# Kernel tuning notes

Measured on AMD Instinct MI355X. Metric: run time of the kernel, lower is better.

The kernel has to match this reference:

```python
import jax, jax.numpy as jnp
import numpy as np

H, W = 192, 640  # image feature-map size (x_rgb[0].shape[2:])


def _pts2img(coor, feat):
    """coor: [N,2] normalized (u,v) in [0,1]; feat: [N,C] -> [C,H,W].
    Mirrors pts2img: swap to (v,u), scale by (H,W), truncate to int,
    last-write-wins scatter into (H+1,W+1,C), crop the overflow row/col."""
    coor = jnp.clip(coor, 0.0, 1.0)
    rc = (coor[:, ::-1] * jnp.array([H, W], coor.dtype)).astype(jnp.int32)  # [N,2] (row,col)
    grid = jnp.zeros((H + 1, W + 1, feat.shape[1]), feat.dtype)
    grid = grid.at[rc[:, 0], rc[:, 1]].set(feat)
    return grid[:H, :W].transpose(2, 0, 1)  # [C,H,W]


def _conv1x1(x, Wm, b):
    # x: [B,C,H,W], Wm: [O,C]
    return jnp.einsum('bchw,oc->bohw', x, Wm) + b[None, :, None, None]


def _conv3x3(x, Wk, b):
    y = jax.lax.conv_general_dilated(x, Wk, window_strides=(1, 1),
                                     padding=((1, 1), (1, 1)),
                                     dimension_numbers=('NCHW', 'OIHW', 'NCHW'))
    return y + b[None, :, None, None]


def setup_inputs() -> dict:
    key = jax.random.key(0)
    ks = jax.random.split(key, 16)
    B, C_IMG = 2, 64
    N0, C0 = 40000, 32
    N1, C1 = 20000, 64
    CL = C1 + 3  # 67
    s = 0.05
    return {
        'x_rgb0': jax.random.normal(ks[0], (B, C_IMG, H, W), jnp.float32),
        'feat0': jax.random.normal(ks[1], (B, N0, C0), jnp.float32),
        'coor0': jax.random.uniform(ks[2], (B, N0, 2), jnp.float32),
        'vox0': jax.random.normal(ks[3], (B, N0, 3), jnp.float32),
        'feat1': jax.random.normal(ks[4], (B, N1, C1), jnp.float32),
        'coor1': jax.random.uniform(ks[5], (B, N1, 2), jnp.float32),
        'vox1': jax.random.normal(ks[6], (B, N1, 3), jnp.float32),
        'W_red0': s * jax.random.normal(ks[7], (CL, C0 + 3), jnp.float32),
        'b_red0': s * jax.random.normal(ks[8], (CL,), jnp.float32),
        'W_red2': s * jax.random.normal(ks[9], (CL, CL), jnp.float32),
        'b_red2': s * jax.random.normal(ks[10], (CL,), jnp.float32),
        'W_red3': s * jax.random.normal(ks[11], (1, C_IMG), jnp.float32),
        'b_red3': s * jax.random.normal(ks[12], (1,), jnp.float32),
        'W_sp': s * jax.random.normal(ks[13], (1, CL, 3, 3), jnp.float32),
        'b_sp': s * jax.random.normal(ks[14], (1,), jnp.float32),
    }


def reference(x_rgb0, feat0, coor0, vox0, feat1, coor1, vox1,
              W_red0, b_red0, W_red2, b_red2, W_red3, b_red3, W_sp, b_sp):
    scatter = jax.vmap(_pts2img)  # over batch
    # level features = cat(sparse features, 3D voxel coords)
    pts_img0 = scatter(coor0, jnp.concatenate([feat0, vox0], axis=-1))  # [B,35,H,W]
    pts_img1 = scatter(coor1, jnp.concatenate([feat1, vox1], axis=-1))  # [B,67,H,W]
    # voxel_idx = [0,1]: 1x1 reduce on level 0, residual add of level 1
    enhanced = _conv1x1(pts_img0, W_red0, b_red0) + pts_img1
    enhanced = _conv1x1(enhanced, W_red2, b_red2)
    gated = _conv1x1(x_rgb0, W_red3, b_red3)  # [B,1,H,W], broadcasts over 67 ch
    fused = gated + enhanced
    att = jax.nn.sigmoid(_conv3x3(fused, W_sp, b_sp))  # [B,1,H,W]
    return x_rgb0 * att
```

## Files before the change

kernel.cpp:

```cpp
#include <hip/hip_runtime.h>
#include <hip/hip_bf16.h>

namespace {
constexpr int kH = 192, kW = 640, kHW = kH * kW;
constexpr int kHW4 = kHW / 4;
constexpr int kB = 2, kC = 64;
constexpr int kN0 = 40000, kC0 = 32;
constexpr int kN1 = 20000, kC1 = 64;
constexpr int kCL = 67;
constexpr int kBHW = kB * kHW;

__global__ void scatter_win(const float* __restrict__ coor0,
                            const float* __restrict__ coor1,
                            int* __restrict__ win0, int* __restrict__ win1) {
  int idx = blockIdx.x * blockDim.x + threadIdx.x;
  const float* coor;
  int* win;
  int N;
  if (idx < kB * kN0) {
    coor = coor0; win = win0; N = kN0;
  } else {
    idx -= kB * kN0;
    if (idx >= kB * kN1) return;
    coor = coor1; win = win1; N = kN1;
  }
  int b = idx / N;
  float u = coor[(size_t)idx * 2 + 0];
  float v = coor[(size_t)idx * 2 + 1];
  u = fminf(fmaxf(u, 0.f), 1.f);
  v = fminf(fmaxf(v, 0.f), 1.f);
  int r = (int)(v * (float)kH);
  int c = (int)(u * (float)kW);
  if (r < kH && c < kW) {
    int n = idx - b * N;
    atomicMax(&win[b * kHW + r * kW + c], n);
  }
}

__global__ __launch_bounds__(640) void kprecomp(
    const float* __restrict__ W0, const float* __restrict__ b0,
    const float* __restrict__ W2, const float* __restrict__ b2,
    const float* __restrict__ Wsp,
    float* __restrict__ M0, float* __restrict__ A1g,
    float* __restrict__ sb, float* __restrict__ wsum) {
  __shared__ float A1s[9 * kCL];
  __shared__ float bp[kCL];
  const int t = threadIdx.x;
  if (t < kCL) {
    float s = b2[t];
    for (int j = 0; j < kCL; ++j) s += W2[t * kCL + j] * b0[j];
    bp[t] = s;
  }
  if (t < 9 * kCL) {
    int k = t / kCL, j = t - k * kCL;
    float s = 0.f;
    for (int c = 0; c < kCL; ++c) s += Wsp[c * 9 + k] * W2[c * kCL + j];
    A1s[t] = s;
    A1g[t] = s;
  }
  __syncthreads();
  if (t < 9 * 35) {
    int k = t / 35, i = t - k * 35;
    float s = 0.f;
    for (int j = 0; j < kCL; ++j) s += A1s[k * kCL + j] * W0[j * 35 + i];
    M0[t] = s;
  }
  if (t >= 576 && t < 585) {
    int k = t - 576;
    float s = 0.f;
    for (int c = 0; c < kCL; ++c) s += Wsp[c * 9 + k] * bp[c];
    sb[k] = s;
  }
  if (t >= 592 && t < 601) {
    int k = t - 592;
    float s = 0.f;
    for (int c = 0; c < kCL; ++c) s += Wsp[c * 9 + k];
    wsum[k] = s;
  }
}

__global__ __launch_bounds__(256) void kgate(const float* __restrict__ x_rgb,
                                             const float* __restrict__ W3,
                                             const float* __restrict__ b3,
                                             float* __restrict__ g) {
  const int j = blockIdx.x * 256 + threadIdx.x;
  const int b = j / kHW4;
  const int p4 = j - b * kHW4;
  const float4* xr = (const float4*)(x_rgb + (size_t)b * kC * kHW) + p4;
  float bias = b3[0];
  float4 acc = make_float4(bias, bias, bias, bias);
#pragma unroll
  for (int c = 0; c < kC; ++c) {
    float wv = W3[c];
    float4 x4 = xr[(size_t)c * kHW4];
    acc.x += wv * x4.x;
    acc.y += wv * x4.y;
    acc.z += wv * x4.z;
    acc.w += wv * x4.w;
  }
  ((float4*)g)[j] = acc;
}

__global__ __launch_bounds__(256) void kgy(
    const float* __restrict__ g,
    const int* __restrict__ win0, const int* __restrict__ win1,
    const float* __restrict__ feat0, const float* __restrict__ vox0,
    const float* __restrict__ feat1, const float* __restrict__ vox1,
    const float* __restrict__ M0, const float* __restrict__ A1,
    const float* __restrict__ sb, const float* __restrict__ wsum,
    float* __restrict__ y) {
  const int pix = blockIdx.x * 256 + threadIdx.x;
  const int b = pix / kHW;
  const float gv = g[pix];
  float yk[9];
#pragma unroll
  for (int k = 0; k < 9; ++k) yk[k] = wsum[k] * gv + sb[k];

  const int w0 = win0[pix];
  if (w0 >= 0) {
    const float* f0 = feat0 + ((size_t)b * kN0 + w0) * kC0;
#pragma unroll
    for (int i = 0; i < kC0; ++i) {
      float v = f0[i];
#pragma unroll
      for (int k = 0; k < 9; ++k) yk[k] += M0[k * 35 + i] * v;
    }
    const float* v0 = vox0 + ((size_t)b * kN0 + w0) * 3;
#pragma unroll
    for (int i = 0; i < 3; ++i) {
      float v = v0[i];
#pragma unroll
      for (int k = 0; k < 9; ++k) yk[k] += M0[k * 35 + kC0 + i] * v;
    }
  }
  const int w1 = win1[pix];
  if (w1 >= 0) {
    const float* f1 = feat1 + ((size_t)b * kN1 + w1) * kC1;
#pragma unroll
    for (int i = 0; i < kC1; ++i) {
      float v = f1[i];
#pragma unroll
      for (int k = 0; k < 9; ++k) yk[k] += A1[k * kCL + i] * v;
    }
    const float* v1 = vox1 + ((size_t)b * kN1 + w1) * 3;
#pragma unroll
    for (int i = 0; i < 3; ++i) {
      float v = v1[i];
#pragma unroll
      for (int k = 0; k < 9; ++k) yk[k] += A1[k * kCL + kC1 + i] * v;
    }
  }
#pragma unroll
  for (int k = 0; k < 9; ++k) y[(size_t)k * kBHW + pix] = yk[k];
}

__global__ __launch_bounds__(256) void katt2(const float* __restrict__ y,
                                             const float* __restrict__ bsp,
                                             float* __restrict__ att) {
  const int pix = blockIdx.x * 256 + threadIdx.x;
  const int b = pix / kHW;
  const int p = pix - b * kHW;
  const int h = p / kW;
  const int w = p - h * kW;

  float logit = bsp[0];
#pragma unroll
  for (int dh = -1; dh <= 1; ++dh) {
    const int hh = h + dh;
    if (hh < 0 || hh >= kH) continue;
#pragma unroll
    for (int dw = -1; dw <= 1; ++dw) {
      const int ww = w + dw;
      if (ww < 0 || ww >= kW) continue;
      const int k = (dh + 1) * 3 + (dw + 1);
      logit += y[(size_t)k * kBHW + b * kHW + hh * kW + ww];
    }
  }
  att[pix] = 1.f / (1.f + __expf(-logit));
}

__global__ __launch_bounds__(256) void kmul(const float* __restrict__ x_rgb,
                                            const float* __restrict__ att,
                                            float* __restrict__ out) {
  const int i = blockIdx.x * 256 + threadIdx.x;
  const int b = i / (kC * kHW4);
  const int r = i - b * (kC * kHW4);
  const int p4 = r % kHW4;
  float4 a4 = ((const float4*)att)[b * kHW4 + p4];
  float4 x4 = ((const float4*)x_rgb)[i];
  x4.x *= a4.x;
  x4.y *= a4.y;
  x4.z *= a4.z;
  x4.w *= a4.w;
  ((float4*)out)[i] = x4;
}

}

extern "C" void kernel_launch(void* const* d_in, const int* in_sizes, int n_in,
                              void* d_out, int out_size, void* d_ws,
                              size_t ws_size, hipStream_t stream) {
  const float* x_rgb = (const float*)d_in[0];
  const float* feat0 = (const float*)d_in[1];
  const float* coor0 = (const float*)d_in[2];
  const float* vox0 = (const float*)d_in[3];
  const float* feat1 = (const float*)d_in[4];
  const float* coor1 = (const float*)d_in[5];
  const float* vox1 = (const float*)d_in[6];
  const float* W0 = (const float*)d_in[7];
  const float* b0 = (const float*)d_in[8];
  const float* W2 = (const float*)d_in[9];
  const float* b2 = (const float*)d_in[10];
  const float* W3 = (const float*)d_in[11];
  const float* b3 = (const float*)d_in[12];
  const float* Wsp = (const float*)d_in[13];
  const float* bsp = (const float*)d_in[14];
  float* out = (float*)d_out;

  float* g = (float*)d_ws;
  float* att = g + (size_t)kBHW;
  float* y = att + (size_t)kBHW;
  int* win0 = (int*)(y + (size_t)9 * kBHW);
  int* win1 = win0 + (size_t)kBHW;
  float* M0 = (float*)(win1 + (size_t)kBHW);
  float* A1 = M0 + 9 * 35;
  float* sb = A1 + 9 * kCL;
  float* wsum = sb + 9;

  hipMemsetAsync(win0, 0xFF, (size_t)2 * kBHW * sizeof(int), stream);
  const int npts = kB * (kN0 + kN1);
  scatter_win<<<(npts + 255) / 256, 256, 0, stream>>>(coor0, coor1, win0,
                                                      win1);
  kprecomp<<<1, 640, 0, stream>>>(W0, b0, W2, b2, Wsp, M0, A1, sb, wsum);
  kgate<<<kB * kHW4 / 256, 256, 0, stream>>>(x_rgb, W3, b3, g);
  kgy<<<kBHW / 256, 256, 0, stream>>>(g, win0, win1, feat0, vox0, feat1, vox1,
                                      M0, A1, sb, wsum, y);
  katt2<<<kBHW / 256, 256, 0, stream>>>(y, bsp, att);
  kmul<<<kB * kC * kHW4 / 256, 256, 0, stream>>>(x_rgb, att, out);
}
```

Before: 76.41 us.

## Fuse gate into y pass, fuse stencil with output multiply, merge setup kernels

Merges the scatter and weight-precompute kernels into one launch and replaces the memset with an init kernel that also zeroes a padded y buffer. The gate reduction is folded into the per-pixel y computation using a shared-memory split over channel quarters. The 3x3 stencil, sigmoid and broadcast multiply are fused into one kernel that reads from the padded buffer without bounds checks. This removes the intermediate g and att round trips and several launches, at the cost of recomputing the stencil four times per pixel group and zeroing a larger padded buffer.

Result: slower. 98.00 us (+28.3%).

```diff
diff --git a/kernel.cpp b/kernel.cpp
--- a/kernel.cpp
+++ b/kernel.cpp
@@ -1,198 +1,237 @@
 #include <hip/hip_runtime.h>
-#include <hip/hip_bf16.h>
 
 namespace {
 constexpr int kH = 192, kW = 640, kHW = kH * kW;
+constexpr int kW4g = kW / 4;
 constexpr int kHW4 = kHW / 4;
 constexpr int kB = 2, kC = 64;
 constexpr int kN0 = 40000, kC0 = 32;
 constexpr int kN1 = 20000, kC1 = 64;
 constexpr int kCL = 67;
 constexpr int kBHW = kB * kHW;
-
-__global__ void scatter_win(const float* __restrict__ coor0,
-                            const float* __restrict__ coor1,
-                            int* __restrict__ win0, int* __restrict__ win1) {
-  int idx = blockIdx.x * blockDim.x + threadIdx.x;
-  const float* coor;
-  int* win;
-  int N;
-  if (idx < kB * kN0) {
-    coor = coor0; win = win0; N = kN0;
+constexpr int kPH = kH + 2, kPW = kW + 8;
+constexpr int kPlane = kPH * kPW;
+constexpr int kYPF = 18 * kPlane;
+constexpr int kYP4 = kYPF / 4;
+constexpr int kWin4 = 2 * kBHW / 4;
+
+__global__ __launch_bounds__(256) void kinit(float4* __restrict__ yp4,
+                                             int4* __restrict__ win4) {
+  int i = blockIdx.x * 256 + threadIdx.x;
+  if (i < kYP4) {
+    yp4[i] = make_float4(0.f, 0.f, 0.f, 0.f);
   } else {
-    idx -= kB * kN0;
-    if (idx >= kB * kN1) return;
-    coor = coor1; win = win1; N = kN1;
-  }
-  int b = idx / N;
-  float u = coor[(size_t)idx * 2 + 0];
-  float v = coor[(size_t)idx * 2 + 1];
-  u = fminf(fmaxf(u, 0.f), 1.f);
-  v = fminf(fmaxf(v, 0.f), 1.f);
-  int r = (int)(v * (float)kH);
-  int c = (int)(u * (float)kW);
-  if (r < kH && c < kW) {
-    int n = idx - b * N;
-    atomicMax(&win[b * kHW + r * kW + c], n);
-  }
-}
-
-__global__ __launch_bounds__(640) void kprecomp(
+    int j = i - kYP4;
+    if (j < kWin4) win4[j] = make_int4(-1, -1, -1, -1);
+  }
+}
+
+__global__ __launch_bounds__(256) void kscatter_precomp(
+    const float* __restrict__ coor0, const float* __restrict__ coor1,
+    int* __restrict__ win0, int* __restrict__ win1,
     const float* __restrict__ W0, const float* __restrict__ b0,
     const float* __restrict__ W2, const float* __restrict__ b2,
-    const float* __restrict__ Wsp,
-    float* __restrict__ M0, float* __restrict__ A1g,
-    float* __restrict__ sb, float* __restrict__ wsum) {
+    const float* __restrict__ Wsp, float* __restrict__ M0,
+    float* __restrict__ A1g, float* __restrict__ sb,
+    float* __restrict__ wsum) {
+  if (blockIdx.x < 469) {
+    int idx = blockIdx.x * 256 + threadIdx.x;
+    const float* coor;
+    int* win;
+    int N;
+    if (idx < kB * kN0) {
+      coor = coor0; win = win0; N = kN0;
+    } else {
+      idx -= kB * kN0;
+      if (idx >= kB * kN1) return;
+      coor = coor1; win = win1; N = kN1;
+    }
+    int b = idx / N;
+    float u = coor[(size_t)idx * 2 + 0];
+    float v = coor[(size_t)idx * 2 + 1];
+    u = fminf(fmaxf(u, 0.f), 1.f);
+    v = fminf(fmaxf(v, 0.f), 1.f);
+    int r = (int)(v * (float)kH);
+    int c = (int)(u * (float)kW);
+    if (r < kH && c < kW) {
+      int n = idx - b * N;
+      atomicMax(&win[b * kHW + r * kW + c], n);
+    }
+    return;
+  }
   __shared__ float A1s[9 * kCL];
-  __shared__ float bp[kCL];
+  __shared__ float bps[kCL];
   const int t = threadIdx.x;
   if (t < kCL) {
     float s = b2[t];
     for (int j = 0; j < kCL; ++j) s += W2[t * kCL + j] * b0[j];
-    bp[t] = s;
-  }
-  if (t < 9 * kCL) {
-    int k = t / kCL, j = t - k * kCL;
+    bps[t] = s;
+  }
+  for (int idx = t; idx < 9 * kCL; idx += 256) {
+    int k = idx / kCL, j = idx - k * kCL;
     float s = 0.f;
     for (int c = 0; c < kCL; ++c) s += Wsp[c * 9 + k] * W2[c * kCL + j];
-    A1s[t] = s;
-    A1g[t] = s;
+    A1s[idx] = s;
+    A1g[idx] = s;
   }
   __syncthreads();
-  if (t < 9 * 35) {
-    int k = t / 35, i = t - k * 35;
+  for (int idx = t; idx < 9 * 35; idx += 256) {
+    int k = idx / 35, i = idx - k * 35;
     float s = 0.f;
     for (int j = 0; j < kCL; ++j) s += A1s[k * kCL + j] * W0[j * 35 + i];
-    M0[t] = s;
-  }
-  if (t >= 576 && t < 585) {
-    int k = t - 576;
-    float s = 0.f;
-    for (int c = 0; c < kCL; ++c) s += Wsp[c * 9 + k] * bp[c];
-    sb[k] = s;
-  }
-  if (t >= 592 && t < 601) {
-    int k = t - 592;
+    M0[idx] = s;
+  }
+  if (t < 9) {
+    float s = 0.f;
+    for (int c = 0; c < kCL; ++c) s += Wsp[c * 9 + t] * bps[c];
+    sb[t] = s;
+  } else if (t >= 16 && t < 25) {
+    int k = t - 16;
     float s = 0.f;
     for (int c = 0; c < kCL; ++c) s += Wsp[c * 9 + k];
     wsum[k] = s;
   }
 }
 
-__global__ __launch_bounds__(256) void kgate(const float* __restrict__ x_rgb,
-                                             const float* __restrict__ W3,
-                                             const float* __restrict__ b3,
-                                             float* __restrict__ g) {
-  const int j = blockIdx.x * 256 + threadIdx.x;
-  const int b = j / kHW4;
-  const int p4 = j - b * kHW4;
-  const float4* xr = (const float4*)(x_rgb + (size_t)b * kC * kHW) + p4;
-  float bias = b3[0];
-  float4 acc = make_float4(bias, bias, bias, bias);
-#pragma unroll
-  for (int c = 0; c < kC; ++c) {
-    float wv = W3[c];
-    float4 x4 = xr[(size_t)c * kHW4];
-    acc.x += wv * x4.x;
-    acc.y += wv * x4.y;
-    acc.z += wv * x4.z;
-    acc.w += wv * x4.w;
-  }
-  ((float4*)g)[j] = acc;
-}
-
-__global__ __launch_bounds__(256) void kgy(
-    const float* __restrict__ g,
-    const int* __restrict__ win0, const int* __restrict__ win1,
-    const float* __restrict__ feat0, const float* __restrict__ vox0,
-    const float* __restrict__ feat1, const float* __restrict__ vox1,
-    const float* __restrict__ M0, const float* __restrict__ A1,
-    const float* __restrict__ sb, const float* __restrict__ wsum,
-    float* __restrict__ y) {
-  const int pix = blockIdx.x * 256 + threadIdx.x;
-  const int b = pix / kHW;
-  const float gv = g[pix];
-  float yk[9];
-#pragma unroll
-  for (int k = 0; k < 9; ++k) yk[k] = wsum[k] * gv + sb[k];
+__global__ __launch_bounds__(256) void kpass1(
+    const float* __restrict__ x_rgb, const int* __restrict__ win0,
+    const int* __restrict__ win1, const float* __restrict__ feat0,
+    const float* __restrict__ vox0, const float* __restrict__ feat1,
+    const float* __restrict__ vox1, const float* __restrict__ M0,
+    const float* __restrict__ A1, const float* __restrict__ sb,
+    const float* __restrict__ wsum, const float* __restrict__ W3,
+    const float* __restrict__ b3, float* __restrict__ yp) {
+  __shared__ float part[64][4][4];
+  const int tid = threadIdx.x;
+  const int P0 = blockIdx.x * 256;
+  const int b = P0 / kHW;
+  {
+    const int g = tid >> 2, q = tid & 3;
+    const int pg = (P0 - b * kHW) / 4 + g;
+    const float4* xr = (const float4*)(x_rgb + (size_t)b * kC * kHW) + pg;
+    float4 acc = make_float4(0.f, 0.f, 0.f, 0.f);
+#pragma unroll
+    for (int cc = 0; cc < 16; ++cc) {
+      const int c = q * 16 + cc;
+      float wv = W3[c];
+      float4 x4 = xr[(size_t)c * kHW4];
+      acc.x += wv * x4.x;
+      acc.y += wv * x4.y;
+      acc.z += wv * x4.z;
+      acc.w += wv * x4.w;
+    }
+    part[g][q][0] = acc.x;
+    part[g][q][1] = acc.y;
+    part[g][q][2] = acc.z;
+    part[g][q][3] = acc.w;
+  }
+  __syncthreads();
+  const int pix = P0 + tid;
+  const int pp = pix - b * kHW;
+  const int h = pp / kW;
+  const int w = pp - h * kW;
+  const int g = tid >> 2, e = tid & 3;
+  const float gv = b3[0] + part[g][0][e] + part[g][1][e] + part[g][2][e] +
+                   part[g][3][e];
+  float y[9];
+#pragma unroll
+  for (int k = 0; k < 9; ++k) y[k] = wsum[k] * gv + sb[k];
 
   const int w0 = win0[pix];
   if (w0 >= 0) {
-    const float* f0 = feat0 + ((size_t)b * kN0 + w0) * kC0;
-#pragma unroll
-    for (int i = 0; i < kC0; ++i) {
-      float v = f0[i];
-#pragma unroll
-      for (int k = 0; k < 9; ++k) yk[k] += M0[k * 35 + i] * v;
+    const float4* f0 = (const float4*)(feat0 + ((size_t)b * kN0 + w0) * kC0);
+#pragma unroll
+    for (int i4 = 0; i4 < 8; ++i4) {
+      float4 v = f0[i4];
+#pragma unroll
+      for (int k = 0; k < 9; ++k) {
+        const float* m = M0 + k * 35 + i4 * 4;
+        y[k] += m[0] * v.x + m[1] * v.y + m[2] * v.z + m[3] * v.w;
+      }
     }
     const float* v0 = vox0 + ((size_t)b * kN0 + w0) * 3;
 #pragma unroll
     for (int i = 0; i < 3; ++i) {
       float v = v0[i];
 #pragma unroll
-      for (int k = 0; k < 9; ++k) yk[k] += M0[k * 35 + kC0 + i] * v;
+      for (int k = 0; k < 9; ++k) y[k] += M0[k * 35 + kC0 + i] * v;
     }
   }
   const int w1 = win1[pix];
   if (w1 >= 0) {
-    const float* f1 = feat1 + ((size_t)b * kN1 + w1) * kC1;
-#pragma unroll
-    for (int i = 0; i < kC1; ++i) {
-      float v = f1[i];
-#pragma unroll
-      for (int k = 0; k < 9; ++k) yk[k] += A1[k * kCL + i] * v;
+    const float4* f1 = (const float4*)(feat1 + ((size_t)b * kN1 + w1) * kC1);
+#pragma unroll
+    for (int i4 = 0; i4 < 16; ++i4) {
+      float4 v = f1[i4];
+#pragma unroll
+      for (int k = 0; k < 9; ++k) {
+        const float* m = A1 + k * kCL + i4 * 4;
+        y[k] += m[0] * v.x + m[1] * v.y + m[2] * v.z + m[3] * v.w;
+      }
     }
     const float* v1 = vox1 + ((size_t)b * kN1 + w1) * 3;
 #pragma unroll
     for (int i = 0; i < 3; ++i) {
       float v = v1[i];
 #pragma unroll
-      for (int k = 0; k < 9; ++k) yk[k] += A1[k * kCL + kC1 + i] * v;
-    }
-  }
-#pragma unroll
-  for (int k = 0; k < 9; ++k) y[(size_t)k * kBHW + pix] = yk[k];
-}
-
-__global__ __launch_bounds__(256) void katt2(const float* __restrict__ y,
-                                             const float* __restrict__ bsp,
-                                             float* __restrict__ att) {
-  const int pix = blockIdx.x * 256 + threadIdx.x;
-  const int b = pix / kHW;
-  const int p = pix - b * kHW;
-  const int h = p / kW;
-  const int w = p - h * kW;
-
-  float logit = bsp[0];
-#pragma unroll
-  for (int dh = -1; dh <= 1; ++dh) {
-    const int hh = h + dh;
-    if (hh < 0 || hh >= kH) continue;
-#pragma unroll
-    for (int dw = -1; dw <= 1; ++dw) {
-      const int ww = w + dw;
-      if (ww < 0 || ww >= kW) continue;
-      const int k = (dh + 1) * 3 + (dw + 1);
-      logit += y[(size_t)k * kBHW + b * kHW + hh * kW + ww];
-    }
-  }
-  att[pix] = 1.f / (1.f + __expf(-logit));
-}
-
-__global__ __launch_bounds__(256) void kmul(const float* __restrict__ x_rgb,
-                                            const float* __restrict__ att,
-                                            float* __restrict__ out) {
-  const int i = blockIdx.x * 256 + threadIdx.x;
-  const int b = i / (kC * kHW4);
-  const int r = i - b * (kC * kHW4);
-  const int p4 = r % kHW4;
-  float4 a4 = ((const float4*)att)[b * kHW4 + p4];
-  float4 x4 = ((const float4*)x_rgb)[i];
-  x4.x *= a4.x;
-  x4.y *= a4.y;
-  x4.z *= a4.z;
-  x4.w *= a4.w;
-  ((float4*)out)[i] = x4;
+      for (int k = 0; k < 9; ++k) y[k] += A1[k * kCL + kC1 + i] * v;
+    }
+  }
+#pragma unroll
+  for (int k = 0; k < 9; ++k) {
+    yp[((size_t)(k * kB + b) * kPH + (h + 1)) * kPW + 4 + w] = y[k];
+  }
+}
+
+__global__ __launch_bounds__(256) void kpass2(const float* __restrict__ x_rgb,
+                                              const float* __restrict__ yp,
+                                              const float* __restrict__ bsp,
+                                              float* __restrict__ out) {
+  const int j = blockIdx.x * 256 + threadIdx.x;
+  const int T = kB * kHW4;
+  const int q = j / T;
+  const int gran = j - q * T;
+  const int b = gran / kHW4;
+  const int p4 = gran - b * kHW4;
+  const int h = p4 / kW4g;
+  const int w4 = p4 - h * kW4g;
+
+  const float bias = bsp[0];
+  float4 lg = make_float4(bias, bias, bias, bias);
+#pragma unroll
+  for (int r = 0; r < 3; ++r) {
+    const size_t rowoff = ((size_t)h + r) * kPW + 4 * w4;
+    const float* pA = yp + (size_t)((3 * r + 0) * kB + b) * kPlane + rowoff;
+    const float* pB = yp + (size_t)((3 * r + 1) * kB + b) * kPlane + rowoff;
+    const float* pC = yp + (size_t)((3 * r + 2) * kB + b) * kPlane + rowoff;
+    float LA = pA[3];
+    float4 a4 = *(const float4*)(pA + 4);
+    float4 b4 = *(const float4*)(pB + 4);
+    float4 c4 = *(const float4*)(pC + 4);
+    float RC = pC[8];
+    lg.x += LA + b4.x + c4.y;
+    lg.y += a4.x + b4.y + c4.z;
+    lg.z += a4.y + b4.z + c4.w;
+    lg.w += a4.z + b4.w + RC;
+  }
+  float4 att;
+  att.x = 1.f / (1.f + __expf(-lg.x));
+  att.y = 1.f / (1.f + __expf(-lg.y));
+  att.z = 1.f / (1.f + __expf(-lg.z));
+  att.w = 1.f / (1.f + __expf(-lg.w));
+
+  const float4* xr = (const float4*)(x_rgb + (size_t)b * kC * kHW) + p4;
+  float4* op = (float4*)(out + (size_t)b * kC * kHW) + p4;
+#pragma unroll
+  for (int cc = 0; cc < 16; ++cc) {
+    const int c = q * 16 + cc;
+    float4 x4 = xr[(size_t)c * kHW4];
+    x4.x *= att.x;
+    x4.y *= att.y;
+    x4.z *= att.z;
+    x4.w *= att.w;
+    op[(size_t)c * kHW4] = x4;
+  }
 }
 
 }
@@ -217,24 +256,19 @@
   const float* bsp = (const float*)d_in[14];
   float* out = (float*)d_out;
 
-  float* g = (float*)d_ws;
-  float* att = g + (size_t)kBHW;
-  float* y = att + (size_t)kBHW;
-  int* win0 = (int*)(y + (size_t)9 * kBHW);
+  float* yp = (float*)d_ws;
+  int* win0 = (int*)(yp + (size_t)kYPF);
   int* win1 = win0 + (size_t)kBHW;
   float* M0 = (float*)(win1 + (size_t)kBHW);
   float* A1 = M0 + 9 * 35;
   float* sb = A1 + 9 * kCL;
   float* wsum = sb + 9;
 
-  hipMemsetAsync(win0, 0xFF, (size_t)2 * kBHW * sizeof(int), stream);
-  const int npts = kB * (kN0 + kN1);
-  scatter_win<<<(npts + 255) / 256, 256, 0, stream>>>(coor0, coor1, win0,
-                                                      win1);
-  kprecomp<<<1, 640, 0, stream>>>(W0, b0, W2, b2, Wsp, M0, A1, sb, wsum);
-  kgate<<<kB * kHW4 / 256, 256, 0, stream>>>(x_rgb, W3, b3, g);
-  kgy<<<kBHW / 256, 256, 0, stream>>>(g, win0, win1, feat0, vox0, feat1, vox1,
-                                      M0, A1, sb, wsum, y);
-  katt2<<<kBHW / 256, 256, 0, stream>>>(y, bsp, att);
-  kmul<<<kB * kC * kHW4 / 256, 256, 0, stream>>>(x_rgb, att, out);
-}
+  const int ninit = kYP4 + kWin4;
+  kinit<<<(ninit + 255) / 256, 256, 0, stream>>>((float4*)yp, (int4*)win0);
+  kscatter_precomp<<<470, 256, 0, stream>>>(coor0, coor1, win0, win1, W0, b0,
+                                            W2, b2, Wsp, M0, A1, sb, wsum);
+  kpass1<<<kBHW / 256, 256, 0, stream>>>(x_rgb, win0, win1, feat0, vox0, feat1,
+                                         vox1, M0, A1, sb, wsum, W3, b3, yp);
+  kpass2<<<kB * kHW4 * 4 / 256, 256, 0, stream>>>(x_rgb, yp, bsp, out);
+}
```
